# Optimization experiments

Hardware: AMD Instinct MI355X
Metric: run time of the kernel (lower is better)

The kernel has to match this reference:

```python
import jax, jax.numpy as jnp
import numpy as np

QMIN, QMAX = -128, 127  # get_quantized_range(8)


def setup_inputs() -> dict:
    key = jax.random.key(0)
    k1, k2, k3, k4 = jax.random.split(key, 4)
    N, IN, OUT = 8192, 4096, 4096
    x = jax.random.randint(k1, (N, IN), QMIN, QMAX + 1, dtype=jnp.int32).astype(jnp.int8)
    weight = jax.random.randint(k2, (OUT, IN), QMIN, QMAX + 1, dtype=jnp.int32).astype(jnp.int8)
    bias = jax.random.randint(k3, (OUT,), -1000, 1000, dtype=jnp.int32)
    weight_scale = jax.random.uniform(k4, (OUT,), dtype=jnp.float32, minval=1e-3, maxval=2e-2)
    return {
        "x": x,
        "weight": weight,
        "bias": bias,
        "weight_scale": weight_scale,
        "input_scale": 0.05,
        "output_scale": 0.1,
        "output_zero_point": -3,
    }


def reference(x, weight, bias, weight_scale, input_scale, output_scale, output_zero_point):
    # int8 GEMM accumulated in int32 (matches CPU path of the torch code)
    acc = jnp.matmul(x.astype(jnp.int32), weight.astype(jnp.int32).T) + bias[None, :]
    # fused per-channel dequant/requant epilogue
    scale = (input_scale * weight_scale / output_scale)[None, :]  # [1, OUT]
    out = acc.astype(jnp.float32) * scale + output_zero_point
    out = jnp.clip(jnp.round(out), QMIN, QMAX).astype(jnp.int8)
    return out
```

## Files before the change

kernel.cpp:

```cpp
#include <hip/hip_runtime.h>
#include <stdint.h>
#include <stddef.h>

typedef int v4i __attribute__((ext_vector_type(4)));

#define GLOAD16(gp, lp) __builtin_amdgcn_global_load_lds( \
    (const __attribute__((address_space(1))) void*)(gp),  \
    (__attribute__((address_space(3))) void*)(lp), 16, 0, 0)

#define PH_BAR()     __builtin_amdgcn_s_barrier()
#define WAIT_VM(n)   asm volatile("s_waitcnt vmcnt(" #n ")" ::: "memory")
#define WAIT_LGKM0() asm volatile("s_waitcnt lgkmcnt(0)" ::: "memory")
#define SCHED_FENCE() __builtin_amdgcn_sched_barrier(0)
#define PRIO1() __builtin_amdgcn_s_setprio(1)
#define PRIO0() __builtin_amdgcn_s_setprio(0)

static __device__ __forceinline__ int pack4(int a, int b, int c, int d) {
    return (a & 255) | ((b & 255) << 8) | ((c & 255) << 16) | (d << 24);
}

__global__ __launch_bounds__(256) void pack2_kernel(const int* __restrict__ srcA, v4i* __restrict__ dstA, int nA,
                                                    const int* __restrict__ srcB, v4i* __restrict__ dstB, int nB) {
    int i = blockIdx.x * blockDim.x + threadIdx.x;
    const int* src; v4i* dst;
    if (i < nA) { src = srcA; dst = dstA; }
    else { i -= nA; if (i >= nB) return; src = srcB; dst = dstB; }
    const v4i* s = reinterpret_cast<const v4i*>(src) + (size_t)i * 4;
    v4i v0 = s[0], v1 = s[1], v2 = s[2], v3 = s[3];
    v4i r;
    r.x = pack4(v0.x, v0.y, v0.z, v0.w);
    r.y = pack4(v1.x, v1.y, v1.z, v1.w);
    r.z = pack4(v2.x, v2.y, v2.z, v2.w);
    r.w = pack4(v3.x, v3.y, v3.z, v3.w);
    dst[i] = r;
}

__global__ __launch_bounds__(512, 1) void gemm_q8_mp(
    const char* __restrict__ Apk, const char* __restrict__ Bpk,
    const int* __restrict__ bias, const float* __restrict__ wscale,
    const float* __restrict__ is_p, const float* __restrict__ os_p,
    const int* __restrict__ zp_p,
    int* __restrict__ out, int K, int Ncols)
{
    __shared__ char lds[131072];

    const int tid  = threadIdx.x;
    const int wid  = tid >> 6;
    const int lane = tid & 63;
    const int l7 = lane & 7, l3 = lane >> 3;
    const int lo16 = lane & 15, hi = lane >> 4;

    int swz;
    {
        const int nwg = gridDim.x;
        const int q = nwg >> 3, r = nwg & 7;
        const int xcd = blockIdx.x & 7;
        const int base = (xcd < r) ? xcd * (q + 1) : r * (q + 1) + (xcd - r) * q;
        swz = base + (blockIdx.x >> 3);
    }
    const int nbc  = Ncols >> 8;
    const int brow = swz / nbc, bcol = swz % nbc;

    const int wr = wid >> 2, wc = wid & 3;

    const char* Ab = Apk + (size_t)(brow * 256 + wid * 8 + l3) * K + ((l7 ^ l3) << 4);
    const char* Bb = Bpk + (size_t)(bcol * 256 + wid * 8 + l3) * K + ((l7 ^ l3) << 4);

    const int colsw0 = (hi ^ l7) << 4;
    const int colsw1 = colsw0 ^ 64;
    const int aBase = (wr << 14) + (lo16 << 7);
    const int bBase = (wc << 13) + (lo16 << 7);

    v4i acc[8][4];
#pragma unroll
    for (int m = 0; m < 8; ++m)
#pragma unroll
        for (int n = 0; n < 4; ++n)
            acc[m][n] = (v4i){0, 0, 0, 0};

    v4i afA[2][2], afB[2][2], bf[4][2];

    auto stage = [&](const char* gb, int ldsOff, int h, int t) {
        const char* g = gb + (size_t)(h * 128) * K + ((size_t)t << 7);
        char* l = lds + (ldsOff + (h << 14) + (wid << 10));
        GLOAD16(g, l);
        GLOAD16(g + (size_t)64 * K, l + 8192);
    };
    auto ldAf = [&](v4i (&dst)[2][2], int bufo, int pair) {
#pragma unroll
        for (int m = 0; m < 2; ++m) {
            const int base = bufo + aBase + (pair << 12) + (m << 11);
            dst[m][0] = *(const v4i*)(lds + base + colsw0);
            dst[m][1] = *(const v4i*)(lds + base + colsw1);
        }
    };
    auto ldBf = [&](int bufo) {
#pragma unroll
        for (int n = 0; n < 4; ++n)
            bf[n][0] = *(const v4i*)(lds + 65536 + bufo + bBase + (n << 11) + colsw0);
#pragma unroll
        for (int n = 0; n < 4; ++n)
            bf[n][1] = *(const v4i*)(lds + 65536 + bufo + bBase + (n << 11) + colsw1);
    };

#define MQ(afX, p) do {                                                           \
    _Pragma("unroll") for (int s_ = 0; s_ < 2; ++s_)                              \
    _Pragma("unroll") for (int m_ = 0; m_ < 2; ++m_)                              \
    _Pragma("unroll") for (int n_ = 0; n_ < 4; ++n_)                              \
        acc[((p) << 1) + m_][n_] = __builtin_amdgcn_mfma_i32_16x16x64_i8(         \
            afX[m_][s_], bf[n_][s_], acc[((p) << 1) + m_][n_], 0, 0, 0);          \
} while (0)

    stage(Ab, 0,     0, 0);  stage(Ab, 0,     1, 0);
    stage(Bb, 65536, 0, 0);  stage(Bb, 65536, 1, 0);
    WAIT_VM(0);
    PH_BAR();
    SCHED_FENCE();
    ldAf(afA, 0, 0);

    const int nt = K >> 7;
    for (int t = 0; t < nt - 1; ++t) {
        const int b  = (t & 1) << 15;
        const int nb = (~t & 1) << 15;

        ldBf(b);
        ldAf(afB, b, 1);
        stage(Ab, nb, 0, t + 1);  stage(Ab, nb, 1, t + 1);
        PRIO1(); MQ(afA, 0); PRIO0();
        ldAf(afA, b, 2);
        stage(Bb, 65536 + nb, 0, t + 1);  stage(Bb, 65536 + nb, 1, t + 1);
        PRIO1(); MQ(afB, 1); PRIO0();
        ldAf(afB, b, 3);
        PRIO1(); MQ(afA, 2); PRIO0();
        WAIT_VM(0);
        WAIT_LGKM0();
        PH_BAR();
        SCHED_FENCE();
        ldAf(afA, nb, 0);
        PRIO1(); MQ(afB, 3); PRIO0();
    }

    {
        const int b = ((nt - 1) & 1) << 15;
        ldBf(b);
        ldAf(afB, b, 1);
        PRIO1(); MQ(afA, 0); PRIO0();
        ldAf(afA, b, 2);
        PRIO1(); MQ(afB, 1); PRIO0();
        ldAf(afB, b, 3);
        PRIO1(); MQ(afA, 2); PRIO0();
        PRIO1(); MQ(afB, 3); PRIO0();
    }
#undef MQ

    const float is = *is_p, os = *os_p;
    const float zp = (float)(*zp_p);
    const int colb = (bcol << 8) + (wc << 6) + lo16;
    float sc[4]; int bv[4];
#pragma unroll
    for (int n = 0; n < 4; ++n) {
        sc[n] = is * wscale[colb + (n << 4)] / os;
        bv[n] = bias[colb + (n << 4)];
    }
#pragma unroll
    for (int m = 0; m < 8; ++m) {
#pragma unroll
        for (int j = 0; j < 4; ++j) {
            const int row = (brow << 8) + (wr << 7) + (m << 4) + (hi << 2) + j;
            int* op = out + (size_t)row * Ncols + colb;
#pragma unroll
            for (int n = 0; n < 4; ++n) {
                float f = (float)(acc[m][n][j] + bv[n]) * sc[n] + zp;
                f = rintf(f);
                f = fminf(fmaxf(f, -128.f), 127.f);
                op[n << 4] = (int)f;
            }
        }
    }
}

template <bool PACKED>
__global__ __launch_bounds__(256) void gemm_q8(
    const void* __restrict__ Ain, const void* __restrict__ Bin,
    const int* __restrict__ bias, const float* __restrict__ wscale,
    const float* __restrict__ is_p, const float* __restrict__ os_p,
    const int* __restrict__ zp_p,
    int* __restrict__ out, int Nrows, int K, int Ncols)
{
    __shared__ char Al[128 * 64];
    __shared__ char Bl[128 * 64];

    const int tid  = threadIdx.x;
    const int wid  = tid >> 6;
    const int lane = tid & 63;

    const int nbc = Ncols / 128;
    int swz = blockIdx.x;
    if ((gridDim.x & 7) == 0) {
        const int cpx = gridDim.x >> 3;
        swz = (blockIdx.x & 7) * cpx + (blockIdx.x >> 3);
    }
    const int brow = swz / nbc;
    const int bcol = swz % nbc;
    const int wr = wid >> 1, wc = wid & 1;

    v4i acc[4][4];
#pragma unroll
    for (int m = 0; m < 4; ++m)
#pragma unroll
        for (int n = 0; n < 4; ++n)
            acc[m][n] = (v4i){0, 0, 0, 0};

    const char* Ag = nullptr;
    const char* Bg = nullptr;
    if (PACKED) {
        Ag = (const char*)Ain + (size_t)(brow * 128 + wid * 32 + (lane >> 2)) * K + (lane & 3) * 16;
        Bg = (const char*)Bin + (size_t)(bcol * 128 + wid * 32 + (lane >> 2)) * K + (lane & 3) * 16;
    }
    char* aldst = Al + wid * 2048;
    char* bldst = Bl + wid * 2048;

    const int lo16 = lane & 15, hi = lane >> 4;
    const int aoff0 = (wr * 64 + lo16) * 64 + hi * 16;
    const int boff0 = (wc * 64 + lo16) * 64 + hi * 16;

    for (int k0 = 0; k0 < K; k0 += 64) {
        if (PACKED) {
            GLOAD16(Ag + k0,          aldst);
            GLOAD16(Ag + 16 * K + k0, aldst + 1024);
            GLOAD16(Bg + k0,          bldst);
            GLOAD16(Bg + 16 * K + k0, bldst + 1024);
        } else {
            const int row = tid >> 1, half = tid & 1;
            const int* sA = (const int*)Ain + (size_t)(brow * 128 + row) * K + k0 + half * 32;
            const int* sB = (const int*)Bin + (size_t)(bcol * 128 + row) * K + k0 + half * 32;
            int pa[8], pb[8];
#pragma unroll
            for (int j = 0; j < 8; ++j) {
                v4i va = reinterpret_cast<const v4i*>(sA)[j];
                v4i vb = reinterpret_cast<const v4i*>(sB)[j];
                pa[j] = pack4(va.x, va.y, va.z, va.w);
                pb[j] = pack4(vb.x, vb.y, vb.z, vb.w);
            }
            v4i* da = (v4i*)&Al[row * 64 + half * 32];
            da[0] = (v4i){pa[0], pa[1], pa[2], pa[3]};
            da[1] = (v4i){pa[4], pa[5], pa[6], pa[7]};
            v4i* db = (v4i*)&Bl[row * 64 + half * 32];
            db[0] = (v4i){pb[0], pb[1], pb[2], pb[3]};
            db[1] = (v4i){pb[4], pb[5], pb[6], pb[7]};
        }
        __syncthreads();

        v4i afr[4], bfr[4];
#pragma unroll
        for (int m = 0; m < 4; ++m)
            afr[m] = *(const v4i*)&Al[aoff0 + m * 16 * 64];
#pragma unroll
        for (int n = 0; n < 4; ++n)
            bfr[n] = *(const v4i*)&Bl[boff0 + n * 16 * 64];
#pragma unroll
        for (int m = 0; m < 4; ++m)
#pragma unroll
            for (int n = 0; n < 4; ++n)
                acc[m][n] = __builtin_amdgcn_mfma_i32_16x16x64_i8(afr[m], bfr[n], acc[m][n], 0, 0, 0);

        __syncthreads();
    }

    const float is = *is_p;
    const float os = *os_p;
    const float zp = (float)(*zp_p);
#pragma unroll
    for (int n = 0; n < 4; ++n) {
        const int col = bcol * 128 + wc * 64 + n * 16 + lo16;
        const float sc = is * wscale[col] / os;
        const int   bv = bias[col];
#pragma unroll
        for (int m = 0; m < 4; ++m) {
            const int row0 = brow * 128 + wr * 64 + m * 16 + hi * 4;
#pragma unroll
            for (int j = 0; j < 4; ++j) {
                float f = (float)(acc[m][n][j] + bv) * sc + zp;
                f = rintf(f);
                f = fminf(fmaxf(f, -128.f), 127.f);
                out[(size_t)(row0 + j) * Ncols + col] = (int)f;
            }
        }
    }
}

extern "C" void kernel_launch(void* const* d_in, const int* in_sizes, int n_in,
                              void* d_out, int out_size, void* d_ws, size_t ws_size,
                              hipStream_t stream) {
    const int*   x32    = (const int*)d_in[0];
    const int*   w32    = (const int*)d_in[1];
    const int*   bias   = (const int*)d_in[2];
    const float* wscale = (const float*)d_in[3];
    const float* isp    = (const float*)d_in[4];
    const float* osp    = (const float*)d_in[5];
    const int*   zpp    = (const int*)d_in[6];
    int* out = (int*)d_out;

    const int OUT = in_sizes[2];
    const int K   = in_sizes[1] / OUT;
    const int Nr  = in_sizes[0] / K;

    const size_t need = (size_t)Nr * K + (size_t)OUT * K;

    if (ws_size >= need) {
        char* xpk = (char*)d_ws;
        char* wpk = xpk + (size_t)Nr * K;
        const int nx16 = (Nr * K) / 16;
        const int nw16 = (OUT * K) / 16;
        pack2_kernel<<<(nx16 + nw16 + 255) / 256, 256, 0, stream>>>(
            x32, (v4i*)xpk, nx16, w32, (v4i*)wpk, nw16);
        if ((Nr & 255) == 0 && (OUT & 255) == 0 && (K & 127) == 0 && (K >> 7) >= 2) {
            const int grid8 = (Nr / 256) * (OUT / 256);
            gemm_q8_mp<<<grid8, 512, 0, stream>>>(xpk, wpk, bias, wscale, isp, osp, zpp,
                                                  out, K, OUT);
        } else {
            const int grid = (Nr / 128) * (OUT / 128);
            gemm_q8<true><<<grid, 256, 0, stream>>>(xpk, wpk, bias, wscale, isp, osp, zpp,
                                                    out, Nr, K, OUT);
        }
    } else {
        const int grid = (Nr / 128) * (OUT / 128);
        gemm_q8<false><<<grid, 256, 0, stream>>>(x32, w32, bias, wscale, isp, osp, zpp,
                                                 out, Nr, K, OUT);
    }
}
```

Baseline: 171.7 us.

## Triple-buffer B tiles in LDS to prefetch two K-steps ahead

Grows LDS to 160KB and gives the B operand three rotating buffers, so B tiles are staged two iterations ahead while A stays double-buffered. The in-loop wait relaxes from vmcnt(0) to vmcnt(4), letting the newest B loads stay in flight across the barrier. This is meant to hide global-load latency for B. In exchange it uses more LDS, requires at least three K tiles, and needs a peeled tail iteration.

```diff
diff --git a/kernel.cpp b/kernel.cpp
--- a/kernel.cpp
+++ b/kernel.cpp
@@ -42,7 +42,7 @@
     const int* __restrict__ zp_p,
     int* __restrict__ out, int K, int Ncols)
 {
-    __shared__ char lds[131072];
+    __shared__ char lds[163840];
 
     const int tid  = threadIdx.x;
     const int wid  = tid >> 6;
@@ -111,43 +111,68 @@
             afX[m_][s_], bf[n_][s_], acc[((p) << 1) + m_][n_], 0, 0, 0);          \
 } while (0)
 
-    stage(Ab, 0,     0, 0);  stage(Ab, 0,     1, 0);
-    stage(Bb, 65536, 0, 0);  stage(Bb, 65536, 1, 0);
-    WAIT_VM(0);
+    stage(Ab, 0,             0, 0);  stage(Ab, 0,             1, 0);
+    stage(Bb, 65536,         0, 0);  stage(Bb, 65536,         1, 0);
+    stage(Bb, 65536 + 32768, 0, 1);  stage(Bb, 65536 + 32768, 1, 1);
+    WAIT_VM(4);
     PH_BAR();
     SCHED_FENCE();
     ldAf(afA, 0, 0);
 
     const int nt = K >> 7;
-    for (int t = 0; t < nt - 1; ++t) {
-        const int b  = (t & 1) << 15;
-        const int nb = (~t & 1) << 15;
-
-        ldBf(b);
-        ldAf(afB, b, 1);
-        stage(Ab, nb, 0, t + 1);  stage(Ab, nb, 1, t + 1);
+    int bcur = 0;
+    for (int t = 0; t < nt - 2; ++t) {
+        const int bA  = (t & 1) << 15;
+        const int nbA = (~t & 1) << 15;
+        int bst = bcur + 65536; if (bst >= 98304) bst -= 98304;
+
+        ldBf(bcur);
+        ldAf(afB, bA, 1);
+        stage(Ab, nbA, 0, t + 1);  stage(Ab, nbA, 1, t + 1);
         PRIO1(); MQ(afA, 0); PRIO0();
-        ldAf(afA, b, 2);
-        stage(Bb, 65536 + nb, 0, t + 1);  stage(Bb, 65536 + nb, 1, t + 1);
+        ldAf(afA, bA, 2);
+        stage(Bb, 65536 + bst, 0, t + 2);  stage(Bb, 65536 + bst, 1, t + 2);
         PRIO1(); MQ(afB, 1); PRIO0();
-        ldAf(afB, b, 3);
+        ldAf(afB, bA, 3);
+        PRIO1(); MQ(afA, 2); PRIO0();
+        WAIT_VM(4);
+        WAIT_LGKM0();
+        PH_BAR();
+        SCHED_FENCE();
+        ldAf(afA, nbA, 0);
+        PRIO1(); MQ(afB, 3); PRIO0();
+
+        bcur += 32768; if (bcur >= 98304) bcur -= 98304;
+    }
+
+    {
+        const int t = nt - 2;
+        const int bA  = (t & 1) << 15;
+        const int nbA = (~t & 1) << 15;
+        ldBf(bcur);
+        ldAf(afB, bA, 1);
+        stage(Ab, nbA, 0, t + 1);  stage(Ab, nbA, 1, t + 1);
+        PRIO1(); MQ(afA, 0); PRIO0();
+        ldAf(afA, bA, 2);
+        PRIO1(); MQ(afB, 1); PRIO0();
+        ldAf(afB, bA, 3);
         PRIO1(); MQ(afA, 2); PRIO0();
         WAIT_VM(0);
         WAIT_LGKM0();
         PH_BAR();
         SCHED_FENCE();
-        ldAf(afA, nb, 0);
+        ldAf(afA, nbA, 0);
         PRIO1(); MQ(afB, 3); PRIO0();
-    }
-
+        bcur += 32768; if (bcur >= 98304) bcur -= 98304;
+    }
     {
-        const int b = ((nt - 1) & 1) << 15;
-        ldBf(b);
-        ldAf(afB, b, 1);
+        const int bA = ((nt - 1) & 1) << 15;
+        ldBf(bcur);
+        ldAf(afB, bA, 1);
         PRIO1(); MQ(afA, 0); PRIO0();
-        ldAf(afA, b, 2);
+        ldAf(afA, bA, 2);
         PRIO1(); MQ(afB, 1); PRIO0();
-        ldAf(afB, b, 3);
+        ldAf(afB, bA, 3);
         PRIO1(); MQ(afA, 2); PRIO0();
         PRIO1(); MQ(afB, 3); PRIO0();
     }
@@ -314,7 +339,7 @@
         const int nw16 = (OUT * K) / 16;
         pack2_kernel<<<(nx16 + nw16 + 255) / 256, 256, 0, stream>>>(
             x32, (v4i*)xpk, nx16, w32, (v4i*)wpk, nw16);
-        if ((Nr & 255) == 0 && (OUT & 255) == 0 && (K & 127) == 0 && (K >> 7) >= 2) {
+        if ((Nr & 255) == 0 && (OUT & 255) == 0 && (K & 127) == 0 && (K >> 7) >= 3) {
             const int grid8 = (Nr / 256) * (OUT / 256);
             gemm_q8_mp<<<grid8, 512, 0, stream>>>(xpk, wpk, bias, wscale, isp, osp, zpp,
                                                   out, K, OUT);
```

After: 169.8 us, median of 2. Within noise of the previous version (-1.1%).
